# Kernel tuning notes

Hardware: AMD Instinct MI355X
Metric: run time of the kernel (lower is better)

## Reference

```python
import jax, jax.numpy as jnp
import numpy as np

D_MODEL = 512
D_IN = D_MODEL * 2          # inner Mamba2 d_model
D_STATE = 128
D_CONV = 4
EXPAND = 2
D_INNER = EXPAND * D_IN     # 2048
HEADDIM = 64
NHEADS = D_INNER // HEADDIM # 32
CONV_DIM = D_INNER + 2 * D_STATE          # x,B,C stream into depthwise conv
D_PROJ = 2 * D_INNER + 2 * D_STATE + NHEADS  # z, xBC, dt
BATCH, SEQ = 2, 4096


def setup_inputs() -> dict:
    key = jax.random.key(0)
    ks = jax.random.split(key, 32)
    r = lambda i, shape, s=1.0: jax.random.normal(ks[i], shape, jnp.float32) * s
    inp = {"x": r(0, (BATCH, SEQ, D_MODEL))}
    inp.update(
        pre_w=r(1, (D_MODEL, D_IN), 0.02), pre_b=jnp.zeros(D_IN, jnp.float32),
        pre_ln_g=jnp.ones(D_IN, jnp.float32), pre_ln_b=jnp.zeros(D_IN, jnp.float32),
        post_w=r(2, (D_IN, D_MODEL), 0.02), post_b=jnp.zeros(D_MODEL, jnp.float32),
        post_ln_g=jnp.ones(D_MODEL, jnp.float32), post_ln_b=jnp.zeros(D_MODEL, jnp.float32),
    )
    for j, m in enumerate(("f", "b")):
        o = 3 + j * 8
        inp[f"win_{m}"] = r(o, (D_IN, D_PROJ), 0.02)
        inp[f"convw_{m}"] = r(o + 1, (CONV_DIM, D_CONV), 0.2)
        inp[f"convb_{m}"] = jnp.zeros(CONV_DIM, jnp.float32)
        inp[f"dtb_{m}"] = r(o + 2, (NHEADS,), 0.1)
        inp[f"Alog_{m}"] = jnp.log(jnp.arange(1, NHEADS + 1, dtype=jnp.float32))
        inp[f"D_{m}"] = jnp.ones(NHEADS, jnp.float32)
        inp[f"normw_{m}"] = jnp.ones(D_INNER, jnp.float32)
        inp[f"wout_{m}"] = r(o + 3, (D_INNER, D_IN), 0.02)
    return inp


def layernorm(x, g, b, eps=1e-5):
    mu = x.mean(-1, keepdims=True)
    v = ((x - mu) ** 2).mean(-1, keepdims=True)
    return (x - mu) * jax.lax.rsqrt(v + eps) * g + b


def dwconv_causal(x, w, b):
    # x: [B,L,C], w: [C,K] depthwise causal conv
    xp = jnp.pad(x, ((0, 0), (D_CONV - 1, 0), (0, 0)))
    y = jax.lax.conv_general_dilated(xp.transpose(0, 2, 1), w[:, None, :], (1,), 'VALID',
                                     feature_group_count=w.shape[0])
    return y.transpose(0, 2, 1) + b


def mamba2(x, win, convw, convb, dtb, Alog, Dp, normw, wout):
    # x: [B,L,D_IN]  ->  [B,L,D_IN]
    zxbcdt = x @ win
    z, xBC, dt = jnp.split(zxbcdt, [D_INNER, D_INNER + CONV_DIM], axis=-1)
    dt = jax.nn.softplus(dt + dtb)                          # [B,L,H]
    xBC = jax.nn.silu(dwconv_causal(xBC, convw, convb))
    xs, Bm, Cm = jnp.split(xBC, [D_INNER, D_INNER + D_STATE], axis=-1)
    xs = xs.reshape(xs.shape[0], xs.shape[1], NHEADS, HEADDIM)  # [B,L,H,P]
    A = -jnp.exp(Alog)                                       # [H]
    decay = jnp.exp(dt * A)                                  # [B,L,H]

    def step(h, inp):
        x_t, B_t, C_t, dt_t, dec_t = inp                     # [B,H,P],[B,N],[B,N],[B,H],[B,H]
        h = h * dec_t[:, :, None, None] + (dt_t[:, :, None] * x_t)[..., None] * B_t[:, None, None, :]
        y_t = jnp.einsum('bhpn,bn->bhp', h, C_t)
        return h, y_t

    h0 = jnp.zeros((x.shape[0], NHEADS, HEADDIM, D_STATE), x.dtype)
    seq = (xs.transpose(1, 0, 2, 3), Bm.transpose(1, 0, 2), Cm.transpose(1, 0, 2),
           dt.transpose(1, 0, 2), decay.transpose(1, 0, 2))
    _, ys = jax.lax.scan(step, h0, seq)                      # ys: [L,B,H,P]
    y = ys.transpose(1, 0, 2, 3) + Dp[None, None, :, None] * xs
    y = y.reshape(y.shape[0], y.shape[1], D_INNER)
    # gated RMSNorm (norm_before_gate=False)
    yg = y * jax.nn.silu(z)
    yn = yg * jax.lax.rsqrt(jnp.mean(yg * yg, -1, keepdims=True) + 1e-5) * normw
    return yn @ wout


def nbimamba2(x, pre_w, pre_b, pre_ln_g, pre_ln_b, post_w, post_b, post_ln_g, post_ln_b,
              win_f, convw_f, convb_f, dtb_f, Alog_f, D_f, normw_f, wout_f,
              win_b, convw_b, convb_b, dtb_b, Alog_b, D_b, normw_b, wout_b):
    shortcut = x
    h = layernorm(x @ pre_w + pre_b, pre_ln_g, pre_ln_b)
    gate = jax.nn.silu(h)
    out_f = mamba2(h, win_f, convw_f, convb_f, dtb_f, Alog_f, D_f, normw_f, wout_f)
    out_b = jnp.flip(mamba2(jnp.flip(h, 1), win_b, convw_b, convb_b, dtb_b, Alog_b, D_b, normw_b, wout_b), 1)
    out = layernorm((out_f * gate + out_b * gate) @ post_w + post_b, post_ln_g, post_ln_b)
    return out + shortcut


def reference(x, pre_w, pre_b, pre_ln_g, pre_ln_b, post_w, post_b, post_ln_g, post_ln_b,
              win_f, convw_f, convb_f, dtb_f, Alog_f, D_f, normw_f, wout_f,
              win_b, convw_b, convb_b, dtb_b, Alog_b, D_b, normw_b, wout_b):
    return nbimamba2(x, pre_w, pre_b, pre_ln_g, pre_ln_b, post_w, post_b, post_ln_g, post_ln_b,
                     win_f, convw_f, convb_f, dtb_f, Alog_f, D_f, normw_f, wout_f,
                     win_b, convw_b, convb_b, dtb_b, Alog_b, D_b, normw_b, wout_b)
```

## Files before the change

kernel.cpp:

```cpp
#include <hip/hip_runtime.h>
#include <stdint.h>

typedef unsigned short u16;
typedef __attribute__((ext_vector_type(8))) short short8;
typedef __attribute__((ext_vector_type(4))) float f32x4;

__device__ __forceinline__ float bf2f(u16 u) {
  union { float f; uint32_t i; } v; v.i = ((uint32_t)u) << 16; return v.f;
}
__device__ __forceinline__ u16 f2bf(float f) {
  union { float f; uint32_t i; } v; v.f = f;
  uint32_t r = v.i + 0x7FFFu + ((v.i >> 16) & 1u);
  return (u16)(r >> 16);
}
__device__ __forceinline__ uint32_t pk2(float a, float b) {
  return (uint32_t)f2bf(a) | ((uint32_t)f2bf(b) << 16);
}
__device__ __forceinline__ void gload16(const u16* g, u16* l) {
  __builtin_amdgcn_global_load_lds(
      (const __attribute__((address_space(1))) unsigned int*)g,
      (__attribute__((address_space(3))) unsigned int*)l, 16, 0, 0);
}

__device__ __forceinline__ float block_sum256(float v) {
  __shared__ float red[4];
  #pragma unroll
  for (int o = 1; o < 64; o <<= 1) v += __shfl_xor(v, o, 64);
  int lane = threadIdx.x & 63, w = threadIdx.x >> 6;
  __syncthreads();
  if (lane == 0) red[w] = v;
  __syncthreads();
  return red[0] + red[1] + red[2] + red[3];
}

__global__ void k_tcast(const float* __restrict__ W, u16* __restrict__ Wt,
                        int K, int N, int Npad) {
  __shared__ float tile[32][33];
  int n0 = blockIdx.x * 32, k0 = blockIdx.y * 32;
  int tx = threadIdx.x, ty0 = threadIdx.y;
  #pragma unroll
  for (int i = 0; i < 4; i++) {
    int ty = ty0 + i * 8;
    int k = k0 + ty, n = n0 + tx;
    tile[ty][tx] = (k < K && n < N) ? W[(size_t)k * N + n] : 0.f;
  }
  __syncthreads();
  #pragma unroll
  for (int i = 0; i < 4; i++) {
    int ty = ty0 + i * 8;
    int n = n0 + ty, k = k0 + tx;
    if (n < Npad && k < K) Wt[(size_t)n * K + k] = f2bf(tile[tx][ty]);
  }
}

__global__ void k_cast(const float* __restrict__ in, u16* __restrict__ out, int n4) {
  int i = blockIdx.x * 256 + threadIdx.x;
  if (i >= n4) return;
  float4 v = ((const float4*)in)[i];
  uint2 o;
  o.x = pk2(v.x, v.y);
  o.y = pk2(v.z, v.w);
  ((uint2*)out)[i] = o;
}

__launch_bounds__(256)
__global__ void k_gemm(const u16* __restrict__ A, const u16* __restrict__ Bt,
                       float* __restrict__ Cf, u16* __restrict__ Cb,
                       const u16* __restrict__ hp,
                       int M, int N, int K, int ldc, int flags) {
  __shared__ u16 lA[2][128 * 64];
  __shared__ u16 lB[2][128 * 64];
  const int tid = threadIdx.x;
  const int lane = tid & 63;
  const int wave = tid >> 6;
  const int bm = blockIdx.x, bn = blockIdx.y;
  const int wr = wave >> 1, wc = wave & 1;
  const int fr = lane & 15, fq = lane >> 4;

  const int srow = wave * 32 + (lane >> 3);
  const int scol = ((lane & 7) ^ (srow & 7)) * 8;
  const u16* gA = A + (size_t)(bm * 128 + srow) * K + scol;
  const u16* gB = Bt + (size_t)(bn * 128 + srow) * K + scol;
  const int lofs = wave * 2048;

  f32x4 acc[4][4] = {};

  #pragma unroll
  for (int i = 0; i < 4; i++) {
    gload16(gA + (size_t)(i * 8) * K, &lA[0][lofs + i * 512]);
    gload16(gB + (size_t)(i * 8) * K, &lB[0][lofs + i * 512]);
  }
  __syncthreads();

  const int NT = K >> 6;
  for (int t = 0; t < NT; ++t) {
    const int cur = t & 1;
    if (t + 1 < NT) {
      const int kt = (t + 1) << 6;
      #pragma unroll
      for (int i = 0; i < 4; i++) {
        gload16(gA + (size_t)(i * 8) * K + kt, &lA[cur ^ 1][lofs + i * 512]);
        gload16(gB + (size_t)(i * 8) * K + kt, &lB[cur ^ 1][lofs + i * 512]);
      }
    }
    #pragma unroll
    for (int kk = 0; kk < 2; kk++) {
      short8 af[4], bfr[4];
      #pragma unroll
      for (int m = 0; m < 4; m++) {
        int row = wr * 64 + m * 16 + fr;
        int sl = (kk * 4 + fq) ^ (row & 7);
        af[m] = *(const short8*)(&lA[cur][row * 64 + sl * 8]);
      }
      #pragma unroll
      for (int n = 0; n < 4; n++) {
        int row = wc * 64 + n * 16 + fr;
        int sl = (kk * 4 + fq) ^ (row & 7);
        bfr[n] = *(const short8*)(&lB[cur][row * 64 + sl * 8]);
      }
      #pragma unroll
      for (int m = 0; m < 4; m++)
        #pragma unroll
        for (int n = 0; n < 4; n++)
          acc[m][n] = __builtin_amdgcn_mfma_f32_16x16x32_bf16(af[m], bfr[n], acc[m][n], 0, 0, 0);
    }
    __syncthreads();
  }

  const bool bf16out = flags & 1, accum = flags & 2, flip = flags & 4, fuse = flags & 8;
  #pragma unroll
  for (int m = 0; m < 4; m++) {
    #pragma unroll
    for (int q = 0; q < 4; q++) {
      int rr = bm * 128 + wr * 64 + m * 16 + fq * 4 + q;
      int orow = flip ? (rr ^ 4095) : rr;
      size_t rb = (size_t)orow * ldc;
      #pragma unroll
      for (int n = 0; n < 4; n++) {
        int cc = bn * 128 + wc * 64 + n * 16 + fr;
        float v = acc[m][n][q];
        if (accum) v += Cf[rb + cc];
        if (fuse) {
          float h = bf2f(hp[rb + cc]);
          v = v * (h / (1.f + __expf(-h)));
        }
        if (bf16out) Cb[rb + cc] = f2bf(v);
        else Cf[rb + cc] = v;
      }
    }
  }
}

__launch_bounds__(512)
__global__ void k_gemm256(const u16* __restrict__ A, const u16* __restrict__ Bt,
                          u16* __restrict__ Cb) {
  constexpr int K = 1024, N = 4480, NT = 16;
  __shared__ u16 lA[2][256 * 64];
  __shared__ u16 lB[2][256 * 64];
  const int tid = threadIdx.x;
  const int lane = tid & 63;
  const int wid = tid >> 6;
  const int bm = blockIdx.x, bn = blockIdx.y;
  const int wr = wid >> 2, wc = wid & 3;
  const int fr = lane & 15, fq = lane >> 4;

  const int srow = tid >> 3;
  const int scol = ((tid & 7) ^ (srow & 7)) * 8;
  const u16* gA[4];
  const u16* gB[4];
  #pragma unroll
  for (int i = 0; i < 4; i++) {
    int arow = bm * 256 + i * 64 + srow;
    gA[i] = A + (size_t)arow * K + scol;
    int brow = bn * 256 + i * 64 + srow;
    if (brow > N - 1) brow = N - 1;
    gB[i] = Bt + (size_t)brow * K + scol;
  }

  f32x4 acc[8][4] = {};

  auto stage = [&](int u) {
    const int buf = u & 1, kt = u << 6;
    #pragma unroll
    for (int i = 0; i < 4; i++)
      gload16(gA[i] + kt, &lA[buf][i * 4096 + tid * 8]);
    #pragma unroll
    for (int i = 0; i < 4; i++)
      gload16(gB[i] + kt, &lB[buf][i * 4096 + tid * 8]);
  };

  stage(0);
  stage(1);
  asm volatile("s_waitcnt vmcnt(8)" ::: "memory");
  __builtin_amdgcn_s_barrier();

  for (int t = 0; t < NT; ++t) {
    const u16* bufA = &lA[t & 1][0];
    const u16* bufB = &lB[t & 1][0];
    #pragma unroll
    for (int kk = 0; kk < 2; kk++) {
      short8 af[8], bfm[4];
      #pragma unroll
      for (int m = 0; m < 8; m++) {
        int row = wr * 128 + m * 16 + fr;
        int sl = (kk * 4 + fq) ^ (row & 7);
        af[m] = *(const short8*)(&bufA[row * 64 + sl * 8]);
      }
      #pragma unroll
      for (int n = 0; n < 4; n++) {
        int row = wc * 64 + n * 16 + fr;
        int sl = (kk * 4 + fq) ^ (row & 7);
        bfm[n] = *(const short8*)(&bufB[row * 64 + sl * 8]);
      }
      #pragma unroll
      for (int m = 0; m < 8; m++)
        #pragma unroll
        for (int n = 0; n < 4; n++)
          acc[m][n] = __builtin_amdgcn_mfma_f32_16x16x32_bf16(af[m], bfm[n], acc[m][n], 0, 0, 0);
    }
    __builtin_amdgcn_s_barrier();
    if (t + 2 < NT) {
      stage(t + 2);
      asm volatile("s_waitcnt vmcnt(8)" ::: "memory");
    } else {
      asm volatile("s_waitcnt vmcnt(0)" ::: "memory");
    }
    __builtin_amdgcn_s_barrier();
  }

  #pragma unroll
  for (int m = 0; m < 8; m++) {
    #pragma unroll
    for (int q = 0; q < 4; q++) {
      size_t rb = (size_t)(bm * 256 + wr * 128 + m * 16 + fq * 4 + q) * N;
      #pragma unroll
      for (int n = 0; n < 4; n++) {
        int cc = bn * 256 + wc * 64 + n * 16 + fr;
        if (cc < N) Cb[rb + cc] = f2bf(acc[m][n][q]);
      }
    }
  }
}

__global__ void k_preln(const float* __restrict__ t, const float* __restrict__ bias,
                        const float* __restrict__ g, const float* __restrict__ bb,
                        u16* __restrict__ out) {
  const int row = blockIdx.x, tid = threadIdx.x;
  float4 v = ((const float4*)(t + (size_t)row * 1024))[tid];
  float4 bi = ((const float4*)bias)[tid];
  float v0 = v.x + bi.x, v1 = v.y + bi.y, v2 = v.z + bi.z, v3 = v.w + bi.w;
  float mean = block_sum256(v0 + v1 + v2 + v3) * (1.f / 1024.f);
  float d0 = v0 - mean, d1 = v1 - mean, d2 = v2 - mean, d3 = v3 - mean;
  float var = block_sum256(d0 * d0 + d1 * d1 + d2 * d2 + d3 * d3) * (1.f / 1024.f);
  float rs = rsqrtf(var + 1e-5f);
  float4 gg = ((const float4*)g)[tid];
  float4 bv = ((const float4*)bb)[tid];
  uint2 o;
  o.x = pk2(d0 * rs * gg.x + bv.x, d1 * rs * gg.y + bv.y);
  o.y = pk2(d2 * rs * gg.z + bv.z, d3 * rs * gg.w + bv.w);
  ((uint2*)(out + (size_t)row * 1024))[tid] = o;
}

__global__ void k_dt2(const u16* __restrict__ zx, const float* __restrict__ dtb,
                      const float* __restrict__ Alog, float* __restrict__ DTt,
                      float* __restrict__ DECt, int flip) {
  int t = blockIdx.x * 256 + threadIdx.x;
  int h = blockIdx.y, b = blockIdx.z;
  int ts = flip ? 4095 - t : t;
  float raw = bf2f(zx[(size_t)((b << 12) + ts) * 4480 + 4352 + h]) + dtb[h];
  float d = (raw > 20.f) ? raw : log1pf(__expf(raw));
  size_t o = (size_t)(b * 32 + h) * 4096 + t;
  DTt[o] = d;
  DECt[o] = __expf(-__expf(Alog[h]) * d);
}

__global__ void k_conv2(const u16* __restrict__ zx, const float* __restrict__ cw,
                        const float* __restrict__ cb, u16* __restrict__ XT,
                        u16* __restrict__ BCtok, u16* __restrict__ BCT, int flip) {
  const int ct = blockIdx.x;
  const int tt = blockIdx.y;
  const int b = blockIdx.z;
  const int tid = threadIdx.x;
  __shared__ float sin_[67][64];
  __shared__ float sout[64][65];
  const int ch0 = ct * 64, t0 = tt * 64;

  for (int i = tid; i < 67 * 16; i += 256) {
    int r = i >> 4, c4 = (i & 15) << 2;
    int tok = t0 - 3 + r;
    float f0 = 0.f, f1 = 0.f, f2 = 0.f, f3 = 0.f;
    if (tok >= 0) {
      int src = (b << 12) + (flip ? 4095 - tok : tok);
      uint2 v = *(const uint2*)(zx + (size_t)src * 4480 + 2048 + ch0 + c4);
      f0 = bf2f((u16)(v.x & 0xFFFF)); f1 = bf2f((u16)(v.x >> 16));
      f2 = bf2f((u16)(v.y & 0xFFFF)); f3 = bf2f((u16)(v.y >> 16));
    }
    sin_[r][c4] = f0; sin_[r][c4 + 1] = f1; sin_[r][c4 + 2] = f2; sin_[r][c4 + 3] = f3;
  }
  __syncthreads();

  const int ch = tid & 63, g = tid >> 6;
  const int chg = ch0 + ch;
  float4 wv = *(const float4*)(cw + (size_t)chg * 4);
  float bias = cb[chg];
  #pragma unroll
  for (int i = 0; i < 16; i++) {
    int tl = g * 16 + i;
    float a = bias + wv.x * sin_[tl][ch] + wv.y * sin_[tl + 1][ch]
                   + wv.z * sin_[tl + 2][ch] + wv.w * sin_[tl + 3][ch];
    sout[tl][ch] = a / (1.f + __expf(-a));
  }
  __syncthreads();

  if (ch0 < 2048) {
    for (int i = tid; i < 64 * 16; i += 256) {
      int chw = i >> 4, t4 = (i & 15) << 2;
      uint2 o;
      o.x = pk2(sout[t4][chw], sout[t4 + 1][chw]);
      o.y = pk2(sout[t4 + 2][chw], sout[t4 + 3][chw]);
      *(uint2*)(XT + ((size_t)(b * 2048 + ch0 + chw)) * 4096 + t0 + t4) = o;
    }
  } else {
    int c2b = (ct - 32) * 64;
    for (int i = tid; i < 64 * 16; i += 256) {
      int chw = i >> 4, t4 = (i & 15) << 2;
      uint2 o;
      o.x = pk2(sout[t4][chw], sout[t4 + 1][chw]);
      o.y = pk2(sout[t4 + 2][chw], sout[t4 + 3][chw]);
      *(uint2*)(BCT + ((size_t)(b * 256 + c2b + chw)) * 4096 + t0 + t4) = o;
    }
    for (int i = tid; i < 64 * 8; i += 256) {
      int r = i >> 3, c8 = (i & 7) << 3;
      uint4 o;
      o.x = pk2(sout[r][c8], sout[r][c8 + 1]);
      o.y = pk2(sout[r][c8 + 2], sout[r][c8 + 3]);
      o.z = pk2(sout[r][c8 + 4], sout[r][c8 + 5]);
      o.w = pk2(sout[r][c8 + 6], sout[r][c8 + 7]);
      *(uint4*)(BCtok + ((size_t)(b * 4096 + t0 + r)) * 256 + c2b + c8) = o;
    }
  }
}

#define NCH 16
#define SWZ(row, oct, msk) (((oct) ^ ((row) & (msk))) << 4)

__device__ __forceinline__ void cumsum256(int tid, int lane, float adt, float dtv,
                                          float* sL, float* sdt, float* spart) {
  float v = adt;
  if (tid < 256) {
    #pragma unroll
    for (int o = 1; o < 64; o <<= 1) {
      float t = __shfl_up(v, o, 64);
      if (lane >= o) v += t;
    }
    if (lane == 63) spart[tid >> 6] = v;
  }
  __syncthreads();
  if (tid < 256) {
    int w = tid >> 6;
    float off = 0.f;
    #pragma unroll
    for (int j = 0; j < 3; j++) if (j < w) off += spart[j];
    sL[tid] = v + off;
    sdt[tid] = dtv;
  }
}

__launch_bounds__(512, 1)
__global__ void k_ssd_a(const u16* __restrict__ XT, const u16* __restrict__ BCT,
                        const float* __restrict__ DTt, const float* __restrict__ Alog,
                        float* __restrict__ HB, float* __restrict__ PR) {
  const int c = blockIdx.x, h = blockIdx.y, b = blockIdx.z;
  const int tid = threadIdx.x;
  const int lane = tid & 63, w = tid >> 6;
  const int fr = lane & 15, fq = lane >> 4;
  const int bh = b * 32 + h;

  __shared__ u16 sX[64 * 256];
  __shared__ u16 sBW[128 * 256];
  __shared__ float sL[256], sdt[256], sw_[256], spart[4];

  float dtv = 0.f;
  if (tid < 256) dtv = DTt[(size_t)bh * 4096 + c * 256 + tid];
  float expA = __expf(Alog[h]);
  cumsum256(tid, lane, -expA * dtv, dtv, sL, sdt, spart);
  __syncthreads();
  if (tid < 256) sw_[tid] = __expf(sL[255] - sL[tid]) * sdt[tid];
  for (int i = tid; i < 2048; i += 512) {
    int p = i >> 5, oct = i & 31;
    uint4 v = *(const uint4*)(XT + ((size_t)(b * 2048 + h * 64 + p) << 12) + c * 256 + oct * 8);
    *(uint4*)((char*)sX + p * 512 + SWZ(p, oct, 15)) = v;
  }
  __syncthreads();
  for (int i = tid; i < 4096; i += 512) {
    int n = i >> 5, oct = i & 31;
    uint4 v = *(const uint4*)(BCT + ((size_t)(b * 256 + n) << 12) + c * 256 + oct * 8);
    const float* swp = sw_ + oct * 8;
    float f0 = bf2f((u16)(v.x & 0xFFFF)) * swp[0];
    float f1 = bf2f((u16)(v.x >> 16)) * swp[1];
    float f2 = bf2f((u16)(v.y & 0xFFFF)) * swp[2];
    float f3 = bf2f((u16)(v.y >> 16)) * swp[3];
    float f4 = bf2f((u16)(v.z & 0xFFFF)) * swp[4];
    float f5 = bf2f((u16)(v.z >> 16)) * swp[5];
    float f6 = bf2f((u16)(v.w & 0xFFFF)) * swp[6];
    float f7 = bf2f((u16)(v.w >> 16)) * swp[7];
    uint4 o;
    o.x = pk2(f0, f1); o.y = pk2(f2, f3); o.z = pk2(f4, f5); o.w = pk2(f6, f7);
    *(uint4*)((char*)sBW + n * 512 + SWZ(n, oct, 15)) = o;
  }
  __syncthreads();

  const int pb = w >> 1, nh = w & 1;
  f32x4 acc[4] = {};
  #pragma unroll
  for (int ks = 0; ks < 8; ks++) {
    int p = pb * 16 + fr;
    short8 af = *(const short8*)((char*)sX + p * 512 + SWZ(p, ks * 4 + fq, 15));
    #pragma unroll
    for (int nb = 0; nb < 4; nb++) {
      int n = nh * 64 + nb * 16 + fr;
      short8 bfm = *(const short8*)((char*)sBW + n * 512 + SWZ(n, ks * 4 + fq, 15));
      acc[nb] = __builtin_amdgcn_mfma_f32_16x16x32_bf16(af, bfm, acc[nb], 0, 0, 0);
    }
  }
  float* hb = HB + (size_t)(bh * NCH + c) * 8192;
  #pragma unroll
  for (int nb = 0; nb < 4; nb++)
    #pragma unroll
    for (int q = 0; q < 4; q++) {
      int p = pb * 16 + fq * 4 + q;
      int n = nh * 64 + nb * 16 + fr;
      hb[p * 128 + n] = acc[nb][q];
    }
  if (tid == 0) PR[bh * NCH + c] = __expf(sL[255]);
}

__global__ void k_scan_b(float* __restrict__ HB, const float* __restrict__ PR) {
  const int eb = blockIdx.x, h = blockIdx.y, b = blockIdx.z;
  const int e = eb * 256 + threadIdx.x;
  const int bh = b * 32 + h;
  float* base = HB + (size_t)bh * NCH * 8192 + e;
  const float* pr = PR + bh * NCH;
  float carry = 0.f;
  #pragma unroll 4
  for (int c = 0; c < NCH; ++c) {
    float v = base[(size_t)c * 8192];
    base[(size_t)c * 8192] = carry;
    carry = pr[c] * carry + v;
  }
}

__launch_bounds__(512, 1)
__global__ void k_ssd_c(const u16* __restrict__ BCtok, const u16* __restrict__ XT,
                        const float* __restrict__ DTt, const float* __restrict__ HB,
                        const float* __restrict__ Alog, const float* __restrict__ Dp,
                        u16* __restrict__ Y) {
  const int c = blockIdx.x, h = blockIdx.y, b = blockIdx.z;
  const int tid = threadIdx.x;
  const int lane = tid & 63, w = tid >> 6;
  const int fr = lane & 15, fq = lane >> 4;
  const int bh = b * 32 + h;
  const size_t m0 = (size_t)b * 4096 + c * 256;

  __shared__ u16 sB[256 * 128];
  __shared__ u16 sX[64 * 256];
  __shared__ u16 sH[64 * 128];
  __shared__ u16 sP[8 * 32 * 64];
  __shared__ float sL[256], sdt[256], spart[4];

  float dtv = 0.f;
  if (tid < 256) dtv = DTt[(size_t)bh * 4096 + c * 256 + tid];
  float expA = __expf(Alog[h]);
  cumsum256(tid, lane, -expA * dtv, dtv, sL, sdt, spart);

  for (int i = tid; i < 4096; i += 512) {
    int tr = i >> 4, oct = i & 15;
    uint4 v = *(const uint4*)(BCtok + ((m0 + tr) << 8) + oct * 8);
    *(uint4*)((char*)sB + tr * 256 + SWZ(tr, oct, 15)) = v;
  }
  for (int i = tid; i < 2048; i += 512) {
    int p = i >> 5, oct = i & 31;
    uint4 v = *(const uint4*)(XT + ((size_t)(b * 2048 + h * 64 + p) << 12) + c * 256 + oct * 8);
    *(uint4*)((char*)sX + p * 512 + SWZ(p, oct, 15)) = v;
  }
  for (int i = tid; i < 1024; i += 512) {
    int p = i >> 4, oct = i & 15;
    const float* src = HB + (size_t)(bh * NCH + c) * 8192 + p * 128 + oct * 8;
    float4 a = *(const float4*)src;
    float4 bb4 = *(const float4*)(src + 4);
    uint4 o;
    o.x = pk2(a.x, a.y); o.y = pk2(a.z, a.w); o.z = pk2(bb4.x, bb4.y); o.w = pk2(bb4.z, bb4.w);
    *(uint4*)((char*)sH + p * 256 + SWZ(p, oct, 15)) = o;
  }
  short8 cf[2][4];
  #pragma unroll
  for (int m = 0; m < 2; m++)
    #pragma unroll
    for (int ks = 0; ks < 4; ks++)
      cf[m][ks] = *(const short8*)(BCtok + ((m0 + w * 32 + m * 16 + fr) << 8) + 128 + ks * 32 + fq * 8);
  __syncthreads();

  float Lt[2][4], eLt[2][4];
  #pragma unroll
  for (int m = 0; m < 2; m++)
    #pragma unroll
    for (int q = 0; q < 4; q++) {
      Lt[m][q] = sL[w * 32 + m * 16 + fq * 4 + q];
      eLt[m][q] = __expf(Lt[m][q]);
    }
  const float Dh = Dp[h];

  f32x4 accY[2][4] = {};
  u16* pw = sP + w * 2048;
  const int ntl = (w >> 1) + 1;
  for (int tt = 0; tt < ntl; tt++) {
    const int t0 = tt * 64;
    f32x4 g[2][4] = {};
    #pragma unroll
    for (int ks = 0; ks < 4; ks++) {
      short8 bfm[4];
      #pragma unroll
      for (int nb = 0; nb < 4; nb++) {
        int tr = t0 + nb * 16 + fr;
        bfm[nb] = *(const short8*)((char*)sB + tr * 256 + SWZ(tr, ks * 4 + fq, 15));
      }
      #pragma unroll
      for (int m = 0; m < 2; m++)
        #pragma unroll
        for (int nb = 0; nb < 4; nb++)
          g[m][nb] = __builtin_amdgcn_mfma_f32_16x16x32_bf16(cf[m][ks], bfm[nb], g[m][nb], 0, 0, 0);
    }
    #pragma unroll
    for (int nb = 0; nb < 4; nb++) {
      int tau = t0 + nb * 16 + fr;
      float Ltau = sL[tau], dtau = sdt[tau];
      #pragma unroll
      for (int m = 0; m < 2; m++) {
        #pragma unroll
        for (int q = 0; q < 4; q++) {
          int t = w * 32 + m * 16 + fq * 4 + q;
          float mask = (tau > t) ? 0.f : __expf(Lt[m][q] - Ltau) * dtau;
          float pv = mask * g[m][nb][q];
          pv = (tau == t) ? pv + Dh : pv;
          int tl = m * 16 + fq * 4 + q, taul = nb * 16 + fr;
          *(u16*)((char*)pw + tl * 128 + ((((taul) >> 3) ^ (tl & 7)) << 4) + (taul & 7) * 2) = f2bf(pv);
        }
      }
    }
    #pragma unroll
    for (int ks = 0; ks < 2; ks++) {
      short8 pf[2], xf[4];
      #pragma unroll
      for (int m = 0; m < 2; m++) {
        int tl = m * 16 + fr;
        pf[m] = *(const short8*)((char*)pw + tl * 128 + (((ks * 4 + fq) ^ (tl & 7)) << 4));
      }
      #pragma unroll
      for (int pb = 0; pb < 4; pb++) {
        int p = pb * 16 + fr;
        int oct = (t0 >> 3) + ks * 4 + fq;
        xf[pb] = *(const short8*)((char*)sX + p * 512 + SWZ(p, oct, 15));
      }
      #pragma unroll
      for (int m = 0; m < 2; m++)
        #pragma unroll
        for (int pb = 0; pb < 4; pb++)
          accY[m][pb] = __builtin_amdgcn_mfma_f32_16x16x32_bf16(pf[m], xf[pb], accY[m][pb], 0, 0, 0);
    }
  }
  f32x4 accO[2][4] = {};
  #pragma unroll
  for (int ks = 0; ks < 4; ks++) {
    short8 hf[4];
    #pragma unroll
    for (int pb = 0; pb < 4; pb++) {
      int p = pb * 16 + fr;
      hf[pb] = *(const short8*)((char*)sH + p * 256 + SWZ(p, ks * 4 + fq, 15));
    }
    #pragma unroll
    for (int m = 0; m < 2; m++)
      #pragma unroll
      for (int pb = 0; pb < 4; pb++)
        accO[m][pb] = __builtin_amdgcn_mfma_f32_16x16x32_bf16(cf[m][ks], hf[pb], accO[m][pb], 0, 0, 0);
  }
  #pragma unroll
  for (int m = 0; m < 2; m++)
    #pragma unroll
    for (int pb = 0; pb < 4; pb++)
      #pragma unroll
      for (int q = 0; q < 4; q++) {
        int t = w * 32 + m * 16 + fq * 4 + q;
        float val = accY[m][pb][q] + eLt[m][q] * accO[m][pb][q];
        Y[(m0 + t) * 2048 + h * 64 + pb * 16 + fr] = f2bf(val);
      }
}

__launch_bounds__(256)
__global__ void k_scan(const u16* __restrict__ XT, const u16* __restrict__ BCtok,
                       const float* __restrict__ DTt, const float* __restrict__ DECt,
                       const float* __restrict__ Dp, u16* __restrict__ y) {
  const int ps = blockIdx.x, h = blockIdx.y, b = blockIdx.z;
  const int tid = threadIdx.x;
  const int tsub = tid & 15, pl = tid >> 4;
  const int p = ps * 16 + pl;
  const u16* xp = XT + ((size_t)(b * 2048 + h * 64 + p)) * 4096;
  const float* dth = DTt + (size_t)(b * 32 + h) * 4096;
  const float* dch = DECt + (size_t)(b * 32 + h) * 4096;
  u16* yp = y + (size_t)b * 4096 * 2048 + h * 64 + p;
  const float Dh = Dp[h];
  float s0 = 0, s1 = 0, s2 = 0, s3 = 0, s4 = 0, s5 = 0, s6 = 0, s7 = 0;
  for (int tau = 0; tau < 4096; ++tau) {
    const u16* bcr = BCtok + ((size_t)(b * 4096 + tau)) * 256;
    uint4 vB = *(const uint4*)(bcr + tsub * 8);
    uint4 vC = *(const uint4*)(bcr + 128 + tsub * 8);
    float xv = bf2f(xp[tau]);
    float a = dth[tau] * xv;
    float dcv = dch[tau];
    s0 = s0 * dcv + a * bf2f((u16)(vB.x & 0xFFFF)); s1 = s1 * dcv + a * bf2f((u16)(vB.x >> 16));
    s2 = s2 * dcv + a * bf2f((u16)(vB.y & 0xFFFF)); s3 = s3 * dcv + a * bf2f((u16)(vB.y >> 16));
    s4 = s4 * dcv + a * bf2f((u16)(vB.z & 0xFFFF)); s5 = s5 * dcv + a * bf2f((u16)(vB.z >> 16));
    s6 = s6 * dcv + a * bf2f((u16)(vB.w & 0xFFFF)); s7 = s7 * dcv + a * bf2f((u16)(vB.w >> 16));
    float sum = s0 * bf2f((u16)(vC.x & 0xFFFF)) + s1 * bf2f((u16)(vC.x >> 16))
              + s2 * bf2f((u16)(vC.y & 0xFFFF)) + s3 * bf2f((u16)(vC.y >> 16))
              + s4 * bf2f((u16)(vC.z & 0xFFFF)) + s5 * bf2f((u16)(vC.z >> 16))
              + s6 * bf2f((u16)(vC.w & 0xFFFF)) + s7 * bf2f((u16)(vC.w >> 16));
    sum += __shfl_xor(sum, 1, 64);
    sum += __shfl_xor(sum, 2, 64);
    sum += __shfl_xor(sum, 4, 64);
    sum += __shfl_xor(sum, 8, 64);
    if (tsub == 0) yp[(size_t)tau * 2048] = f2bf(sum + Dh * xv);
  }
}

__global__ void k_gate(const u16* __restrict__ y, const u16* __restrict__ zx,
                       const float* __restrict__ normw, u16* __restrict__ u, int flip) {
  const int m = blockIdx.x, tid = threadIdx.x;
  const int ms = flip ? (m ^ 4095) : m;
  uint4 yv = *(const uint4*)(y + (size_t)m * 2048 + tid * 8);
  uint4 zv = *(const uint4*)(zx + (size_t)ms * 4480 + tid * 8);
  const u16* yp = (const u16*)&yv;
  const u16* zp = (const u16*)&zv;
  float vals[8];
  float ss = 0.f;
  #pragma unroll
  for (int i = 0; i < 8; i++) {
    float zf = bf2f(zp[i]);
    float wv = bf2f(yp[i]) * (zf / (1.f + __expf(-zf)));
    vals[i] = wv;
    ss += wv * wv;
  }
  float rs = rsqrtf(block_sum256(ss) * (1.f / 2048.f) + 1e-5f);
  float4 n0 = *(const float4*)(normw + tid * 8);
  float4 n1 = *(const float4*)(normw + tid * 8 + 4);
  uint4 o;
  o.x = pk2(vals[0] * rs * n0.x, vals[1] * rs * n0.y);
  o.y = pk2(vals[2] * rs * n0.z, vals[3] * rs * n0.w);
  o.z = pk2(vals[4] * rs * n1.x, vals[5] * rs * n1.y);
  o.w = pk2(vals[6] * rs * n1.z, vals[7] * rs * n1.w);
  *(uint4*)(u + (size_t)m * 2048 + tid * 8) = o;
}

__global__ void k_final(const float* __restrict__ t2, const float* __restrict__ bias,
                        const float* __restrict__ g, const float* __restrict__ bb,
                        const float* __restrict__ x, float* __restrict__ out) {
  const int row = blockIdx.x, tid = threadIdx.x;
  float2 v = ((const float2*)(t2 + (size_t)row * 512))[tid];
  float v0 = v.x + bias[tid * 2], v1 = v.y + bias[tid * 2 + 1];
  float mean = block_sum256(v0 + v1) * (1.f / 512.f);
  float d0 = v0 - mean, d1 = v1 - mean;
  float var = block_sum256(d0 * d0 + d1 * d1) * (1.f / 512.f);
  float rs = rsqrtf(var + 1e-5f);
  float2 xr = ((const float2*)(x + (size_t)row * 512))[tid];
  float2 o;
  o.x = d0 * rs * g[tid * 2] + bb[tid * 2] + xr.x;
  o.y = d1 * rs * g[tid * 2 + 1] + bb[tid * 2 + 1] + xr.y;
  ((float2*)(out + (size_t)row * 512))[tid] = o;
}

extern "C" void kernel_launch(void* const* d_in, const int* in_sizes, int n_in,
                              void* d_out, int out_size, void* d_ws, size_t ws_size,
                              hipStream_t stream) {
  const float* x      = (const float*)d_in[0];
  const float* pre_w  = (const float*)d_in[1];
  const float* pre_b  = (const float*)d_in[2];
  const float* pre_g  = (const float*)d_in[3];
  const float* pre_bb = (const float*)d_in[4];
  const float* post_w = (const float*)d_in[5];
  const float* post_b = (const float*)d_in[6];
  const float* post_g = (const float*)d_in[7];
  const float* post_bb= (const float*)d_in[8];
  const float* win_[2]   = {(const float*)d_in[9],  (const float*)d_in[17]};
  const float* convw_[2] = {(const float*)d_in[10], (const float*)d_in[18]};
  const float* convb_[2] = {(const float*)d_in[11], (const float*)d_in[19]};
  const float* dtb_[2]   = {(const float*)d_in[12], (const float*)d_in[20]};
  const float* Alog_[2]  = {(const float*)d_in[13], (const float*)d_in[21]};
  const float* Dp_[2]    = {(const float*)d_in[14], (const float*)d_in[22]};
  const float* normw_[2] = {(const float*)d_in[15], (const float*)d_in[23]};
  const float* wout_[2]  = {(const float*)d_in[16], (const float*)d_in[24]};

  char* ws = (char*)d_ws;
  constexpr size_t OFF_WT_PRE  = 0;
  constexpr size_t OFF_WT_WINF = OFF_WT_PRE  + 1048576;
  constexpr size_t OFF_WT_WINB = OFF_WT_WINF + 9175040;
  constexpr size_t OFF_WT_WOF  = OFF_WT_WINB + 9175040;
  constexpr size_t OFF_WT_WOB  = OFF_WT_WOF  + 4194304;
  constexpr size_t OFF_WT_POST = OFF_WT_WOB  + 4194304;
  constexpr size_t OFF_HPRE    = OFF_WT_POST + 1048576;
  constexpr size_t OFF_ZX      = OFF_HPRE + 16777216;
  constexpr size_t OFF_XT      = OFF_ZX + 73400320;
  constexpr size_t OFF_BC      = OFF_XT + 33554432;
  constexpr size_t OFF_DT      = OFF_BC + 8388608;
  constexpr size_t OFF_DEC     = OFF_DT + 1048576;
  constexpr size_t OFF_Y       = OFF_DEC + 1048576;
  constexpr size_t OFF_S       = OFF_Y + 33554432;
  constexpr size_t OFF_HB      = OFF_S + 33554432;
  constexpr size_t ARENA_END   = OFF_HB + 33554432;

  u16* WtPre    = (u16*)(ws + OFF_WT_PRE);
  u16* WtWin[2] = {(u16*)(ws + OFF_WT_WINF), (u16*)(ws + OFF_WT_WINB)};
  u16* WtWo[2]  = {(u16*)(ws + OFF_WT_WOF),  (u16*)(ws + OFF_WT_WOB)};
  u16* WtPost   = (u16*)(ws + OFF_WT_POST);
  u16* HPRE = (u16*)(ws + OFF_HPRE);
  u16* ZX   = (u16*)(ws + OFF_ZX);
  u16* XT   = (u16*)(ws + OFF_XT);
  u16* BCtok= (u16*)(ws + OFF_BC);
  u16* BCT  = (u16*)(ws + OFF_BC + 4194304);
  float* DTt = (float*)(ws + OFF_DT);
  float* DECt= (float*)(ws + OFF_DEC);
  u16*  Y   = (u16*)(ws + OFF_Y);
  float* S  = (float*)(ws + OFF_S);
  float* HB = (float*)(ws + OFF_HB);
  float* PRb  = (float*)(ws + OFF_WT_PRE);
  u16*   XBF  = (u16*)(ws + OFF_Y);
  float* TMP  = S;
  u16*   U    = (u16*)(ws + OFF_XT);
  u16*   U2   = ZX;
  float* TMP2 = (float*)(ws + OFF_XT);

  const bool chunked = (ws_size >= ARENA_END);

  dim3 tb(32, 8);
  k_tcast<<<dim3(32, 16),  tb, 0, stream>>>(pre_w,   WtPre,    512, 1024, 1024);
  k_tcast<<<dim3(140, 32), tb, 0, stream>>>(win_[0], WtWin[0], 1024, 4384, 4480);
  k_tcast<<<dim3(140, 32), tb, 0, stream>>>(win_[1], WtWin[1], 1024, 4384, 4480);
  k_tcast<<<dim3(32, 64),  tb, 0, stream>>>(wout_[0], WtWo[0], 2048, 1024, 1024);
  k_tcast<<<dim3(32, 64),  tb, 0, stream>>>(wout_[1], WtWo[1], 2048, 1024, 1024);
  k_tcast<<<dim3(16, 32),  tb, 0, stream>>>(post_w,  WtPost,   1024,  512,  512);
  k_cast<<<4096, 256, 0, stream>>>(x, XBF, 1048576);
  k_gemm<<<dim3(64, 8), 256, 0, stream>>>(XBF, WtPre, TMP, nullptr, nullptr,
                                          8192, 1024, 512, 1024, 0);
  k_preln<<<8192, 256, 0, stream>>>(TMP, pre_b, pre_g, pre_bb, HPRE);

  for (int d = 0; d < 2; d++) {
    int flip = d;
    k_gemm256<<<dim3(32, 18), 512, 0, stream>>>(HPRE, WtWin[d], ZX);
    k_dt2<<<dim3(16, 32, 2), 256, 0, stream>>>(ZX, dtb_[d], Alog_[d], DTt, DECt, flip);
    k_conv2<<<dim3(36, 64, 2), 256, 0, stream>>>(ZX, convw_[d], convb_[d], XT, BCtok, BCT, flip);
    if (chunked) {
      k_ssd_a<<<dim3(NCH, 32, 2), 512, 0, stream>>>(XT, BCT, DTt, Alog_[d], HB, PRb);
      k_scan_b<<<dim3(32, 32, 2), 256, 0, stream>>>(HB, PRb);
      k_ssd_c<<<dim3(NCH, 32, 2), 512, 0, stream>>>(BCtok, XT, DTt, HB, Alog_[d], Dp_[d], Y);
    } else {
      k_scan<<<dim3(4, 32, 2), 256, 0, stream>>>(XT, BCtok, DTt, DECt, Dp_[d], Y);
    }
    k_gate<<<8192, 256, 0, stream>>>(Y, ZX, normw_[d], U, flip);
    if (d == 0) {
      k_gemm<<<dim3(64, 8), 256, 0, stream>>>(U, WtWo[d], S, nullptr, nullptr,
                                              8192, 1024, 2048, 1024, 0);
    } else {
      k_gemm<<<dim3(64, 8), 256, 0, stream>>>(U, WtWo[d], S, U2, HPRE,
                                              8192, 1024, 2048, 1024, 1 | 2 | 4 | 8);
    }
  }

  k_gemm<<<dim3(64, 4), 256, 0, stream>>>(U2, WtPost, TMP2, nullptr, nullptr,
                                          8192, 512, 1024, 512, 0);
  k_final<<<8192, 256, 0, stream>>>(TMP2, post_b, post_g, post_bb, x, (float*)d_out);
}
```

Baseline: 723.3 us.

## Halve GEMM K-tile to 32, remap LDS swizzle, add grouped block-ID remapping

The 256x256 in-projection GEMM now stages K-tiles of 32 instead of 64. That halves the LDS footprint per buffer and doubles the number of pipeline iterations, with a new paired-row swizzle layout for the LDS reads. Block indices are also remapped so that consecutive workgroups are spread across groups of 8, intended to improve L2 reuse of A and B tiles. The smaller LDS use may allow higher occupancy, at the cost of more barriers per unit of work.

New measurement: 780.4 us. 7.9% more time.

```diff
diff --git a/kernel.cpp b/kernel.cpp
--- a/kernel.cpp
+++ b/kernel.cpp
@@ -154,74 +154,67 @@
 __launch_bounds__(512)
 __global__ void k_gemm256(const u16* __restrict__ A, const u16* __restrict__ Bt,
                           u16* __restrict__ Cb) {
-  constexpr int K = 1024, N = 4480, NT = 16;
-  __shared__ u16 lA[2][256 * 64];
-  __shared__ u16 lB[2][256 * 64];
+  constexpr int K = 1024, N = 4480, NT = 32;
+  __shared__ u16 lA[2][256 * 32];
+  __shared__ u16 lB[2][256 * 32];
   const int tid = threadIdx.x;
   const int lane = tid & 63;
   const int wid = tid >> 6;
-  const int bm = blockIdx.x, bn = blockIdx.y;
+  const int wgid = blockIdx.y * 32 + blockIdx.x;
+  const int nid = (wgid & 7) * 72 + (wgid >> 3);
+  const int bm = nid & 31, bn = nid >> 5;
   const int wr = wid >> 2, wc = wid & 3;
   const int fr = lane & 15, fq = lane >> 4;
 
-  const int srow = tid >> 3;
-  const int scol = ((tid & 7) ^ (srow & 7)) * 8;
-  const u16* gA[4];
-  const u16* gB[4];
-  #pragma unroll
-  for (int i = 0; i < 4; i++) {
-    int arow = bm * 256 + i * 64 + srow;
-    gA[i] = A + (size_t)arow * K + scol;
-    int brow = bn * 256 + i * 64 + srow;
-    if (brow > N - 1) brow = N - 1;
-    gB[i] = Bt + (size_t)brow * K + scol;
-  }
+  const int srow = 2 * (tid >> 3) + ((tid >> 2) & 1);
+  const int scol = ((tid & 3) ^ ((tid >> 3) & 3)) * 8;
+  const u16* gA0 = A + (size_t)(bm * 256 + srow) * K + scol;
+  const u16* gA1 = gA0 + (size_t)128 * K;
+  int br0 = bn * 256 + srow;       if (br0 > N - 1) br0 = N - 1;
+  int br1 = bn * 256 + 128 + srow; if (br1 > N - 1) br1 = N - 1;
+  const u16* gB0 = Bt + (size_t)br0 * K + scol;
+  const u16* gB1 = Bt + (size_t)br1 * K + scol;
 
   f32x4 acc[8][4] = {};
 
   auto stage = [&](int u) {
-    const int buf = u & 1, kt = u << 6;
-    #pragma unroll
-    for (int i = 0; i < 4; i++)
-      gload16(gA[i] + kt, &lA[buf][i * 4096 + tid * 8]);
-    #pragma unroll
-    for (int i = 0; i < 4; i++)
-      gload16(gB[i] + kt, &lB[buf][i * 4096 + tid * 8]);
+    const int buf = u & 1, kt = u << 5;
+    gload16(gA0 + kt, &lA[buf][tid * 8]);
+    gload16(gA1 + kt, &lA[buf][4096 + tid * 8]);
+    gload16(gB0 + kt, &lB[buf][tid * 8]);
+    gload16(gB1 + kt, &lB[buf][4096 + tid * 8]);
   };
 
   stage(0);
   stage(1);
-  asm volatile("s_waitcnt vmcnt(8)" ::: "memory");
+  asm volatile("s_waitcnt vmcnt(4)" ::: "memory");
   __builtin_amdgcn_s_barrier();
 
   for (int t = 0; t < NT; ++t) {
     const u16* bufA = &lA[t & 1][0];
     const u16* bufB = &lB[t & 1][0];
-    #pragma unroll
-    for (int kk = 0; kk < 2; kk++) {
-      short8 af[8], bfm[4];
-      #pragma unroll
-      for (int m = 0; m < 8; m++) {
-        int row = wr * 128 + m * 16 + fr;
-        int sl = (kk * 4 + fq) ^ (row & 7);
-        af[m] = *(const short8*)(&bufA[row * 64 + sl * 8]);
-      }
-      #pragma unroll
-      for (int n = 0; n < 4; n++) {
-        int row = wc * 64 + n * 16 + fr;
-        int sl = (kk * 4 + fq) ^ (row & 7);
-        bfm[n] = *(const short8*)(&bufB[row * 64 + sl * 8]);
-      }
-      #pragma unroll
-      for (int m = 0; m < 8; m++)
-        #pragma unroll
-        for (int n = 0; n < 4; n++)
-          acc[m][n] = __builtin_amdgcn_mfma_f32_16x16x32_bf16(af[m], bfm[n], acc[m][n], 0, 0, 0);
-    }
+    short8 af[8], bfm[4];
+    #pragma unroll
+    for (int m = 0; m < 8; m++) {
+      int row = wr * 128 + m * 16 + fr;
+      int off = ((row >> 1) << 6) + ((row & 1) << 5) + ((fq ^ ((row >> 1) & 3)) << 3);
+      af[m] = *(const short8*)(&bufA[off]);
+    }
+    #pragma unroll
+    for (int n = 0; n < 4; n++) {
+      int row = wc * 64 + n * 16 + fr;
+      int off = ((row >> 1) << 6) + ((row & 1) << 5) + ((fq ^ ((row >> 1) & 3)) << 3);
+      bfm[n] = *(const short8*)(&bufB[off]);
+    }
+    #pragma unroll
+    for (int m = 0; m < 8; m++)
+      #pragma unroll
+      for (int n = 0; n < 4; n++)
+        acc[m][n] = __builtin_amdgcn_mfma_f32_16x16x32_bf16(af[m], bfm[n], acc[m][n], 0, 0, 0);
     __builtin_amdgcn_s_barrier();
     if (t + 2 < NT) {
       stage(t + 2);
-      asm volatile("s_waitcnt vmcnt(8)" ::: "memory");
+      asm volatile("s_waitcnt vmcnt(4)" ::: "memory");
     } else {
       asm volatile("s_waitcnt vmcnt(0)" ::: "memory");
     }
```
